# Kernel optimization log

Hardware: AMD Instinct MI355X
Metric: run time of the kernel (lower is better)

Reference implementation:

```python
import jax, jax.numpy as jnp
import numpy as np

B, M, D = 2, 8192, 2
N = (64, 64)


def setup_inputs() -> dict:
    key = jax.random.key(0)
    k1, k2 = jax.random.split(key)
    # non-uniform sample points in [-0.5, 0.5)^D
    x = jax.random.uniform(k1, (B, M, D), dtype=jnp.float32) - 0.5
    f_hat = jax.random.normal(k2, (B,) + N, dtype=jnp.float32)
    return {"x": x, "f_hat": f_hat}


def reference(x, f_hat):
    # frequency index grid: cartesian product of arange(-Ni//2, Ni//2) -> [K, D]
    Ns = f_hat.shape[1:]
    grids = [jnp.arange(-(n // 2), n - n // 2, dtype=x.dtype) for n in Ns]
    inds = jnp.stack(jnp.meshgrid(*grids, indexing="ij"), axis=-1).reshape(-1, len(Ns))  # [K, D]
    # phase[b, m, k] = <inds[k], x[b, m]>
    phase = jnp.einsum("bmd,kd->bmk", x, inds)
    fourier = jnp.exp(-2j * jnp.pi * phase)  # [B, M, K] complex64 (the huge intermediate)
    fh = f_hat.reshape(f_hat.shape[0], -1).astype(fourier.dtype)  # [B, K]
    y = jnp.einsum("bmk,bk->bm", fourier, fh)  # [B, M] complex64
    return y
```

## Files before the change

### kernel.cpp

```cpp
#include <hip/hip_runtime.h>
#include <math.h>


#define TWO_PI 6.28318530717958647692f
#define BM 16384

__global__ __launch_bounds__(512) void ndft_kernel(
    const float* __restrict__ x,
    const float* __restrict__ f_hat,
    float* __restrict__ out,
    int planar)
{
    __shared__ float fh[64 * 64];
    __shared__ float part[8][64][2];

    const int t   = threadIdx.x;
    const int sub = t >> 6;
    const int lp  = t & 63;
    const int gp  = blockIdx.x * 64 + lp;
    const int b   = gp >> 13;

    {
        const float4* src = (const float4*)(f_hat + b * 4096);
        float4* dst = (float4*)fh;
        dst[t]       = src[t];
        dst[t + 512] = src[t + 512];
    }
    __syncthreads();

    const float2 xp = ((const float2*)x)[gp];
    const float x1 = xp.x, x2 = xp.y;

    float s2, c2;
    sincosf(TWO_PI * x2, &s2, &c2);
    const float twoc = 2.0f * c2;

    float s1, c1;
    sincosf(TWO_PI * x1, &s1, &c1);

    const int k1base = sub << 3;
    float Pr, Pi;
    {
        const float theta = fmaf(-TWO_PI * (float)(k1base - 32), x1,
                                 (32.0f * TWO_PI) * x2);
        sincosf(theta, &Pi, &Pr);
    }

    float yr = 0.0f, yi = 0.0f;

    for (int pr2 = 0; pr2 < 4; ++pr2) {
        const int k1 = k1base + (pr2 << 1);
        const float4* f0 = (const float4*)(fh + (k1 << 6));
        const float4* f1 = (const float4*)(fh + ((k1 + 1) << 6));

        float u1a = 0.0f, u2a = 0.0f;
        float u1b = 0.0f, u2b = 0.0f;

        #pragma unroll
        for (int q = 15; q >= 0; --q) {
            const float4 fa = f0[q];
            const float4 fb = f1[q];
            {
                const float A = fmaf(twoc, u1a, fa.w - u2a);
                const float B = fmaf(twoc, A,   fa.z - u1a);
                const float C = fmaf(twoc, B,   fa.y - A);
                const float D = fmaf(twoc, C,   fa.x - B);
                u2a = C; u1a = D;
            }
            {
                const float A = fmaf(twoc, u1b, fb.w - u2b);
                const float B = fmaf(twoc, A,   fb.z - u1b);
                const float C = fmaf(twoc, B,   fb.y - A);
                const float D = fmaf(twoc, C,   fb.x - B);
                u2b = C; u1b = D;
            }
        }

        const float Sra = fmaf(-c2, u2a, u1a);
        const float Sia = -s2 * u2a;
        const float Srb = fmaf(-c2, u2b, u1b);
        const float Sib = -s2 * u2b;

        yr = fmaf(Pr, Sra, fmaf(-Pi, Sia, yr));
        yi = fmaf(Pr, Sia, fmaf( Pi, Sra, yi));
        {
            const float nPr = fmaf(Pr, c1,  Pi * s1);
            const float nPi = fmaf(Pi, c1, -Pr * s1);
            Pr = nPr; Pi = nPi;
        }
        yr = fmaf(Pr, Srb, fmaf(-Pi, Sib, yr));
        yi = fmaf(Pr, Sib, fmaf( Pi, Srb, yi));
        {
            const float nPr = fmaf(Pr, c1,  Pi * s1);
            const float nPi = fmaf(Pi, c1, -Pr * s1);
            Pr = nPr; Pi = nPi;
        }
    }

    part[sub][lp][0] = yr;
    part[sub][lp][1] = yi;
    __syncthreads();

    if (t < 128) {
        const int p = t >> 1, comp = t & 1;
        float s = 0.0f;
        #pragma unroll
        for (int w = 0; w < 8; ++w) s += part[w][p][comp];
        const int g = blockIdx.x * 64 + p;
        if (planar) {
            out[comp * BM + g] = s;
        } else if (comp == 0) {
            out[g] = s;
        }
    }
}

extern "C" void kernel_launch(void* const* d_in, const int* in_sizes, int n_in,
                              void* d_out, int out_size, void* d_ws, size_t ws_size,
                              hipStream_t stream) {
    const float* x     = (const float*)d_in[0];
    const float* f_hat = (const float*)d_in[1];
    float* out = (float*)d_out;

    const int planar = (out_size >= 2 * BM) ? 1 : 0;

    ndft_kernel<<<dim3(256), dim3(512), 0, stream>>>(x, f_hat, out, planar);
}
```

Measured before the change: 59.80 us.

## Split k1 rows across more threads and use hardware sin/cos intrinsics

Each thread now handles one pair of k1 rows instead of four pairs, so blocks become 1024 threads covering 32 points and the grid doubles to 512 blocks. The per-point reduction grows to 32 partial sums. Library sincosf calls are replaced with __builtin_amdgcn_sinf/cosf on range-reduced turns (fractional part of x), which removes the expensive argument reduction. The aim is more parallelism and less transcendental overhead, at the cost of more shared-memory partial sums, more redundant per-thread setup, and the lower accuracy of the hardware sin/cos.

Measured after the change: 58.62 us. 2.0% less time.

```diff
diff --git a/kernel.cpp b/kernel.cpp
--- a/kernel.cpp
+++ b/kernel.cpp
@@ -2,111 +2,101 @@
 #include <math.h>
 
 
-#define TWO_PI 6.28318530717958647692f
 #define BM 16384
 
-__global__ __launch_bounds__(512) void ndft_kernel(
+__global__ __launch_bounds__(1024, 8) void ndft_kernel(
     const float* __restrict__ x,
     const float* __restrict__ f_hat,
     float* __restrict__ out,
     int planar)
 {
     __shared__ float fh[64 * 64];
-    __shared__ float part[8][64][2];
+    __shared__ float part[32][32][2];
 
-    const int t   = threadIdx.x;
-    const int sub = t >> 6;
-    const int lp  = t & 63;
-    const int gp  = blockIdx.x * 64 + lp;
-    const int b   = gp >> 13;
+    const int t     = threadIdx.x;
+    const int lane  = t & 63;
+    const int wv    = t >> 6;
+    const int pt    = lane & 31;
+    const int half  = lane >> 5;
+    const int chunk = (wv << 1) | half;
+    const int k1a   = chunk << 1;
+
+    const int gp = blockIdx.x * 32 + pt;
+    const int b  = gp >> 13;
 
     {
         const float4* src = (const float4*)(f_hat + b * 4096);
-        float4* dst = (float4*)fh;
-        dst[t]       = src[t];
-        dst[t + 512] = src[t + 512];
+        ((float4*)fh)[t] = src[t];
     }
     __syncthreads();
 
     const float2 xp = ((const float2*)x)[gp];
     const float x1 = xp.x, x2 = xp.y;
 
-    float s2, c2;
-    sincosf(TWO_PI * x2, &s2, &c2);
+    const float u2r = x2 - floorf(x2);
+    const float s2  = __builtin_amdgcn_sinf(u2r);
+    const float c2  = __builtin_amdgcn_cosf(u2r);
     const float twoc = 2.0f * c2;
 
-    float s1, c1;
-    sincosf(TWO_PI * x1, &s1, &c1);
+    const float u1r = x1 - floorf(x1);
+    const float s1  = __builtin_amdgcn_sinf(u1r);
+    const float c1  = __builtin_amdgcn_cosf(u1r);
 
-    const int k1base = sub << 3;
-    float Pr, Pi;
-    {
-        const float theta = fmaf(-TWO_PI * (float)(k1base - 32), x1,
-                                 (32.0f * TWO_PI) * x2);
-        sincosf(theta, &Pi, &Pr);
-    }
+    float uP = (float)(32 - k1a) * x1 + 32.0f * x2;
+    uP -= floorf(uP);
+    const float Pi_ = __builtin_amdgcn_sinf(uP);
+    const float Pr_ = __builtin_amdgcn_cosf(uP);
 
-    float yr = 0.0f, yi = 0.0f;
+    const float4* f0 = (const float4*)(fh + (k1a << 6));
+    const float4* f1 = (const float4*)(fh + ((k1a + 1) << 6));
 
-    for (int pr2 = 0; pr2 < 4; ++pr2) {
-        const int k1 = k1base + (pr2 << 1);
-        const float4* f0 = (const float4*)(fh + (k1 << 6));
-        const float4* f1 = (const float4*)(fh + ((k1 + 1) << 6));
+    float u1a = 0.0f, u2a = 0.0f;
+    float u1b = 0.0f, u2b = 0.0f;
 
-        float u1a = 0.0f, u2a = 0.0f;
-        float u1b = 0.0f, u2b = 0.0f;
-
-        #pragma unroll
-        for (int q = 15; q >= 0; --q) {
-            const float4 fa = f0[q];
-            const float4 fb = f1[q];
-            {
-                const float A = fmaf(twoc, u1a, fa.w - u2a);
-                const float B = fmaf(twoc, A,   fa.z - u1a);
-                const float C = fmaf(twoc, B,   fa.y - A);
-                const float D = fmaf(twoc, C,   fa.x - B);
-                u2a = C; u1a = D;
-            }
-            {
-                const float A = fmaf(twoc, u1b, fb.w - u2b);
-                const float B = fmaf(twoc, A,   fb.z - u1b);
-                const float C = fmaf(twoc, B,   fb.y - A);
-                const float D = fmaf(twoc, C,   fb.x - B);
-                u2b = C; u1b = D;
-            }
+    #pragma unroll
+    for (int q = 15; q >= 0; --q) {
+        const float4 fa = f0[q];
+        const float4 fb = f1[q];
+        {
+            const float A = fmaf(twoc, u1a, fa.w - u2a);
+            const float B = fmaf(twoc, A,   fa.z - u1a);
+            const float C = fmaf(twoc, B,   fa.y - A);
+            const float D = fmaf(twoc, C,   fa.x - B);
+            u2a = C; u1a = D;
         }
-
-        const float Sra = fmaf(-c2, u2a, u1a);
-        const float Sia = -s2 * u2a;
-        const float Srb = fmaf(-c2, u2b, u1b);
-        const float Sib = -s2 * u2b;
-
-        yr = fmaf(Pr, Sra, fmaf(-Pi, Sia, yr));
-        yi = fmaf(Pr, Sia, fmaf( Pi, Sra, yi));
         {
-            const float nPr = fmaf(Pr, c1,  Pi * s1);
-            const float nPi = fmaf(Pi, c1, -Pr * s1);
-            Pr = nPr; Pi = nPi;
-        }
-        yr = fmaf(Pr, Srb, fmaf(-Pi, Sib, yr));
-        yi = fmaf(Pr, Sib, fmaf( Pi, Srb, yi));
-        {
-            const float nPr = fmaf(Pr, c1,  Pi * s1);
-            const float nPi = fmaf(Pi, c1, -Pr * s1);
-            Pr = nPr; Pi = nPi;
+            const float A = fmaf(twoc, u1b, fb.w - u2b);
+            const float B = fmaf(twoc, A,   fb.z - u1b);
+            const float C = fmaf(twoc, B,   fb.y - A);
+            const float D = fmaf(twoc, C,   fb.x - B);
+            u2b = C; u1b = D;
         }
     }
 
-    part[sub][lp][0] = yr;
-    part[sub][lp][1] = yi;
+    const float Sra = fmaf(-c2, u2a, u1a);
+    const float Sia = -s2 * u2a;
+    const float Srb = fmaf(-c2, u2b, u1b);
+    const float Sib = -s2 * u2b;
+
+    const float Pbr = fmaf(Pr_, c1,  Pi_ * s1);
+    const float Pbi = fmaf(Pi_, c1, -Pr_ * s1);
+
+    float yr, yi;
+    yr = fmaf(Pr_, Sra, -Pi_ * Sia);
+    yi = fmaf(Pr_, Sia,  Pi_ * Sra);
+    yr = fmaf(Pbr, Srb, fmaf(-Pbi, Sib, yr));
+    yi = fmaf(Pbr, Sib, fmaf( Pbi, Srb, yi));
+
+    part[chunk][pt][0] = yr;
+    part[chunk][pt][1] = yi;
     __syncthreads();
 
-    if (t < 128) {
+    if (t < 64) {
         const int p = t >> 1, comp = t & 1;
         float s = 0.0f;
         #pragma unroll
-        for (int w = 0; w < 8; ++w) s += part[w][p][comp];
-        const int g = blockIdx.x * 64 + p;
+        for (int w = 0; w < 32; ++w) s += part[w][p][comp];
+        const int g = blockIdx.x * 32 + p;
         if (planar) {
             out[comp * BM + g] = s;
         } else if (comp == 0) {
@@ -124,5 +114,5 @@
 
     const int planar = (out_size >= 2 * BM) ? 1 : 0;
 
-    ndft_kernel<<<dim3(256), dim3(512), 0, stream>>>(x, f_hat, out, planar);
+    ndft_kernel<<<dim3(512), dim3(1024), 0, stream>>>(x, f_hat, out, planar);
 }
```
